# Kernel tuning notes

Measured on AMD Instinct MI355X. Metric: run time of the kernel, lower is better.

Reference implementation:

```python
import jax, jax.numpy as jnp
import numpy as np

NUM_GROUPS = 10
BN_EPS = 1e-5


def _conv1d(x, w, b):
    # x: [B, C, L], w: [O, I, K], 'same' padding
    y = jax.lax.conv_general_dilated(x, w, window_strides=(1,), padding='SAME',
                                     dimension_numbers=('NCH', 'OIH', 'NCH'))
    return y + b[None, :, None]


def _batchnorm1d(x, gamma, beta):
    # training-mode batch statistics over (batch, length) per channel
    mean = jnp.mean(x, axis=(0, 2), keepdims=True)
    var = jnp.var(x, axis=(0, 2), keepdims=True)
    return (x - mean) * jax.lax.rsqrt(var + BN_EPS) * gamma[None, :, None] + beta[None, :, None]


def _conv_block(x, cw, cb, g, b, rw=None, rb=None):
    residual = x if rw is None else _conv1d(x, rw, rb)
    y = jax.nn.relu(_batchnorm1d(_conv1d(x, cw, cb), g, b))
    return y + residual  # dropout is identity at inference


def setup_inputs() -> dict:
    key = jax.random.key(0)
    ks = jax.random.split(key, 16)
    B, N, F, H, G, C = 64, 4096, 512, 64, NUM_GROUPS, 2
    s = lambda k, shp, fan: jax.random.normal(k, shp, jnp.float32) * (1.0 / np.sqrt(fan))
    return {
        'x':    jax.random.normal(ks[0], (B, N, F), jnp.float32),
        'Wd':   s(ks[1], (F, H), F),   'bd':  jnp.zeros((H,), jnp.float32),
        'Wa1':  s(ks[2], (H, H // 2), H), 'ba1': jnp.zeros((H // 2,), jnp.float32),
        'Wa2':  s(ks[3], (H // 2, 1), H // 2), 'ba2': jnp.zeros((1,), jnp.float32),
        'c1w':  s(ks[4], (H, G, 3), G * 3), 'c1b': jnp.zeros((H,), jnp.float32),
        'bn1g': jnp.ones((H,), jnp.float32), 'bn1b': jnp.zeros((H,), jnp.float32),
        'r1w':  s(ks[5], (H, G, 1), G), 'r1b': jnp.zeros((H,), jnp.float32),
        'c2w':  s(ks[6], (H, H, 3), H * 3), 'c2b': jnp.zeros((H,), jnp.float32),
        'bn2g': jnp.ones((H,), jnp.float32), 'bn2b': jnp.zeros((H,), jnp.float32),
        'Wc':   s(ks[7], (H, C), H), 'bc': jnp.zeros((C,), jnp.float32),
    }


def reference(x, Wd, bd, Wa1, ba1, Wa2, ba2, c1w, c1b, bn1g, bn1b, r1w, r1b,
              c2w, c2b, bn2g, bn2b, Wc, bc):
    B, N, _ = x.shape
    h = x @ Wd + bd                                   # [B, N, H]
    # lightweight patch attention
    scores = jnp.tanh(h @ Wa1 + ba1) @ Wa2 + ba2      # [B, N, 1]
    mask = (jnp.sum(jnp.abs(h), axis=2, keepdims=True) > 0).astype(h.dtype)
    scores = scores * mask - 1e10 * (1.0 - mask)
    attn = jax.nn.softmax(scores, axis=1)             # [B, N, 1]
    weighted = h * attn                               # [B, N, H]
    # segment-sum patches into fixed contiguous groups
    ppg = (N + NUM_GROUPS - 1) // NUM_GROUPS
    seg = jnp.arange(N) // ppg                        # [N]
    onehot = jax.nn.one_hot(seg, NUM_GROUPS, dtype=h.dtype)  # [N, G]
    grouped = jnp.einsum('bnh,ng->bgh', weighted, onehot)    # [B, G, H]
    # conv stack on [B, G(channels), H(length)]
    y = _conv_block(grouped, c1w, c1b, bn1g, bn1b, r1w, r1b)
    y = _conv_block(y, c2w, c2b, bn2g, bn2b)
    pooled = jnp.mean(y, axis=2)                      # [B, H] global avg pool
    logits = pooled @ Wc + bc                         # [B, 2]
    return logits
```

## Files before the change

### kernel.cpp

```cpp
#include <hip/hip_runtime.h>
#include <math.h>

#define B_   64
#define N_   4096
#define F_   512
#define H_   64
#define G_   10
#define PPG_ 410

typedef __attribute__((ext_vector_type(8))) short short8v;
typedef __attribute__((ext_vector_type(16))) float f32x16;

__device__ __forceinline__ unsigned short f2bf(float f) {
    union { float f; unsigned int u; } v; v.f = f;
    const unsigned int u = v.u;
    return (unsigned short)((u + 0x7FFFu + ((u >> 16) & 1u)) >> 16);
}
__device__ __forceinline__ float bf2f(unsigned short u) {
    union { unsigned int u; float f; } v; v.u = ((unsigned int)u) << 16;
    return v.f;
}
__device__ __forceinline__ float fast_tanh(float x) {
    return 1.f - 2.f / (__expf(2.f * x) + 1.f);
}

static const size_t OFF_H    = 0;
static const size_t OFF_PNUM = 16777216;
static const size_t OFF_PDEN = OFF_PNUM + 524288;
static const size_t OFF_B1P  = OFF_PDEN + 4096;
static const size_t OFF_B1Q  = OFF_B1P + 4096;
static const size_t OFF_B2P  = OFF_B1Q + 4096;
static const size_t OFF_B2Q  = OFF_B2P + 4096;
static const size_t OFF_Y1   = OFF_B2Q + 4096;
static const size_t OFF_RES1 = OFF_Y1  + 262144;
static const size_t OFF_Z1   = OFF_RES1+ 262144;
static const size_t OFF_Y2   = OFF_Z1  + 262144;
static const size_t OFF_WDT  = OFF_Y2  + 262144;

__global__ __launch_bounds__(256) void k0_wdt(const float* __restrict__ Wd,
                                              unsigned short* __restrict__ WdT)
{
    const int t = blockIdx.x * 256 + threadIdx.x;
    const int k = t >> 6, c = t & 63;
    WdT[((size_t)c << 9) + k] = f2bf(Wd[t]);
}

__global__ __launch_bounds__(256) void k1_gemm(
    const float* __restrict__ x, const unsigned short* __restrict__ WdT,
    const float* __restrict__ bd, unsigned short* __restrict__ h)
{
    __shared__ __align__(16) unsigned char atile[2 * 8192];
    __shared__ __align__(16) unsigned char btile[65536];

    const int tid = threadIdx.x;
    const int w   = tid >> 6;
    const int l   = tid & 63;
    const int rowb = (w >> 1) << 5;
    const int lc  = l & 31;
    const int kh  = l >> 5;

    #pragma unroll
    for (int i = 0; i < 16; ++i) {
        const int p = i * 4096 + tid * 16;
        short8v v = *(const short8v*)((const unsigned char*)WdT + p);
        const int col = p >> 10;
        const int k0  = (p >> 1) & 511;
        const int j   = k0 >> 4;
        const int khh = (k0 >> 3) & 1;
        const int dst = ((j << 1) + (col >> 5)) * 1024 + ((khh << 5) + (col & 31)) * 16;
        *(short8v*)(btile + dst) = v;
    }

    const int srow = tid >> 2;
    const int sq   = tid & 3;
    int wo[4];
    #pragma unroll
    for (int j = 0; j < 4; ++j)
        wo[j] = srow * 128 + ((((j << 1) + (sq >> 1)) ^ (srow & 7)) << 4) + ((sq & 1) << 3);

    const int rb  = (rowb + lc) * 128;
    const int rx7 = lc & 7;
    const unsigned char* bbase = btile + (w & 1) * 1024;

    const int mt0 = blockIdx.x * 8;

    #pragma unroll 1
    for (int mt = 0; mt < 8; ++mt) {
        const int m0 = (mt0 + mt) * 64;
        const float* sp = x + (size_t)(m0 + srow) * F_ + sq * 4;

        f32x16 acc;
        #pragma unroll
        for (int i = 0; i < 16; ++i) acc[i] = 0.f;

        float4 px[4];
        #pragma unroll
        for (int j = 0; j < 4; ++j) px[j] = *(const float4*)(sp + j * 16);
        #pragma unroll
        for (int j = 0; j < 4; ++j) {
            ushort4 v;
            v.x = f2bf(px[j].x); v.y = f2bf(px[j].y);
            v.z = f2bf(px[j].z); v.w = f2bf(px[j].w);
            *(ushort4*)(atile + wo[j]) = v;
        }
        __syncthreads();

        int cur = 0;
        #pragma unroll 1
        for (int t = 0; t < 8; ++t) {
            if (t < 7) {
                const float* q = sp + (t + 1) * 64;
                #pragma unroll
                for (int j = 0; j < 4; ++j) px[j] = *(const float4*)(q + j * 16);
            }
            const unsigned char* ab = atile + cur * 8192;
            #pragma unroll
            for (int s = 0; s < 4; ++s) {
                short8v a = *(const short8v*)(ab + rb + (((kh + 2 * s) ^ rx7) << 4));
                short8v b = *(const short8v*)(bbase + (((t * 4 + s) << 1)) * 1024 + l * 16);
                acc = __builtin_amdgcn_mfma_f32_32x32x16_bf16(a, b, acc, 0, 0, 0);
            }
            if (t < 7) {
                unsigned char* wbuf = atile + (cur ^ 1) * 8192;
                #pragma unroll
                for (int j = 0; j < 4; ++j) {
                    ushort4 v;
                    v.x = f2bf(px[j].x); v.y = f2bf(px[j].y);
                    v.z = f2bf(px[j].z); v.w = f2bf(px[j].w);
                    *(ushort4*)(wbuf + wo[j]) = v;
                }
            }
            __syncthreads();
            cur ^= 1;
        }

        const int col = ((w & 1) << 5) + lc;
        const float bcol = bd[col];
        unsigned short* hb = h + (size_t)m0 * H_;
        #pragma unroll
        for (int r = 0; r < 16; ++r) {
            const int row = rowb + (r & 3) + ((r >> 2) << 3) + (kh << 2);
            hb[(size_t)row * H_ + col] = f2bf(acc[r] + bcol);
        }
    }
}

__global__ __launch_bounds__(256) void k2a_scores(
    const unsigned short* __restrict__ h,
    const float* __restrict__ Wa1, const float* __restrict__ ba1,
    const float* __restrict__ Wa2, const float* __restrict__ ba2,
    float* __restrict__ pnum, float* __restrict__ pden)
{
    __shared__ __align__(16) float rowbuf[64][68];
    __shared__ __align__(16) float was[2048];
    __shared__ float bas[32], wa2s[32];
    __shared__ float sexp[64];
    __shared__ float rnum[4][2][64];

    const int p = blockIdx.x, tid = threadIdx.x;
    for (int i = tid; i < 2048; i += 256) was[i] = Wa1[i];
    if (tid < 32) { bas[tid] = ba1[tid]; wa2s[tid] = Wa2[tid]; }

    const int sr = tid >> 2;
    const int q  = tid & 3;
    const int j0 = q * 8;
    const size_t n0 = (size_t)p * 64;

    {
        const unsigned short* src = h + (n0 + sr) * H_ + q * 16;
        short8v v0 = *(const short8v*)(src);
        short8v v1 = *(const short8v*)(src + 8);
        float* dst = &rowbuf[sr][q * 16];
        float4 f0, f1, f2, f3;
        f0.x = bf2f((unsigned short)v0[0]); f0.y = bf2f((unsigned short)v0[1]);
        f0.z = bf2f((unsigned short)v0[2]); f0.w = bf2f((unsigned short)v0[3]);
        f1.x = bf2f((unsigned short)v0[4]); f1.y = bf2f((unsigned short)v0[5]);
        f1.z = bf2f((unsigned short)v0[6]); f1.w = bf2f((unsigned short)v0[7]);
        f2.x = bf2f((unsigned short)v1[0]); f2.y = bf2f((unsigned short)v1[1]);
        f2.z = bf2f((unsigned short)v1[2]); f2.w = bf2f((unsigned short)v1[3]);
        f3.x = bf2f((unsigned short)v1[4]); f3.y = bf2f((unsigned short)v1[5]);
        f3.z = bf2f((unsigned short)v1[6]); f3.w = bf2f((unsigned short)v1[7]);
        *(float4*)(dst)      = f0;
        *(float4*)(dst + 4)  = f1;
        *(float4*)(dst + 8)  = f2;
        *(float4*)(dst + 12) = f3;
    }
    __syncthreads();

    const float4* was4 = (const float4*)was;
    float tac[8];
    #pragma unroll
    for (int u = 0; u < 8; ++u) tac[u] = bas[j0 + u];
    for (int k = 0; k < 64; ++k) {
        const float hv = rowbuf[sr][k];
        const float4 wa = was4[k * 8 + (q << 1)];
        const float4 wb = was4[k * 8 + (q << 1) + 1];
        tac[0] += hv * wa.x; tac[1] += hv * wa.y;
        tac[2] += hv * wa.z; tac[3] += hv * wa.w;
        tac[4] += hv * wb.x; tac[5] += hv * wb.y;
        tac[6] += hv * wb.z; tac[7] += hv * wb.w;
    }
    float part = 0.f;
    #pragma unroll
    for (int u = 0; u < 8; ++u) part += fast_tanh(tac[u]) * wa2s[j0 + u];
    float sa = 0.f;
    for (int k = q * 16; k < q * 16 + 16; ++k) sa += fabsf(rowbuf[sr][k]);
    part += __shfl_xor(part, 1);
    part += __shfl_xor(part, 2);
    sa   += __shfl_xor(sa, 1);
    sa   += __shfl_xor(sa, 2);
    if (q == 0) sexp[sr] = (sa > 0.f) ? __expf(part + ba2[0]) : 0.f;
    __syncthreads();

    if (tid < 64) {
        float e = sexp[tid];
        #pragma unroll
        for (int o = 1; o < 64; o <<= 1) e += __shfl_xor(e, o);
        if (tid == 0) pden[p] = e;
    }

    const int pl   = p & 63;
    const int nb0  = pl * 64;
    const int glo  = nb0 / PPG_;
    const int col  = tid & 63, qq = tid >> 6;
    float acc0 = 0.f, acc1 = 0.f;
    for (int r = qq; r < 64; r += 4) {
        const float e = sexp[r];
        const float v = rowbuf[r][col];
        if ((nb0 + r) / PPG_ == glo) acc0 += e * v; else acc1 += e * v;
    }
    rnum[qq][0][col] = acc0;
    rnum[qq][1][col] = acc1;
    __syncthreads();
    if (tid < 128) {
        const int slot = tid >> 6, c2 = tid & 63;
        pnum[((size_t)p * 2 + slot) * 64 + c2] =
            rnum[0][slot][c2] + rnum[1][slot][c2] + rnum[2][slot][c2] + rnum[3][slot][c2];
    }
}

__global__ __launch_bounds__(256) void k4_conv1(
    const float* __restrict__ pnum, const float* __restrict__ pden,
    const float* __restrict__ c1w, const float* __restrict__ c1b,
    const float* __restrict__ r1w, const float* __restrict__ r1b,
    float* __restrict__ y1raw, float* __restrict__ res1,
    float* __restrict__ b1p, float* __restrict__ b1q)
{
    __shared__ __align__(16) float gs[G_][68];
    __shared__ float cws[30 * 64];
    __shared__ float rws[G_ * 64];
    __shared__ float c1bs[64], r1bs[64];
    __shared__ float red[256];
    __shared__ float dsh;

    const int b = blockIdx.x, tid = threadIdx.x;

    if (tid < 64) {
        float e = pden[b * 64 + tid];
        #pragma unroll
        for (int o = 1; o < 64; o <<= 1) e += __shfl_xor(e, o);
        if (tid == 0) dsh = e;
    }
    for (int i = tid; i < 30 * 64; i += 256) {
        const int ik = i >> 6, o = i & 63;
        cws[i] = c1w[o * 30 + ik];
    }
    for (int i = tid; i < G_ * 64; i += 256) {
        const int ch = i >> 6, o = i & 63;
        rws[i] = r1w[o * G_ + ch];
    }
    if (tid < 64) { c1bs[tid] = c1b[tid]; r1bs[tid] = r1b[tid]; }
    if (tid < G_) { gs[tid][0] = 0.f; gs[tid][65] = 0.f; gs[tid][66] = 0.f; gs[tid][67] = 0.f; }
    __syncthreads();

    const float inv = 1.f / dsh;
    for (int i = tid; i < 640; i += 256) {
        const int ch = i >> 6, col = i & 63;
        int p_lo = (PPG_ * ch) >> 6;
        int p_hi = (PPG_ * (ch + 1) - 1) >> 6;
        if (p_hi > 63) p_hi = 63;
        float acc = 0.f;
        for (int pl = p_lo; pl <= p_hi; ++pl) {
            const int glo = (pl * 64) / PPG_;
            const int slot = (glo == ch) ? 0 : 1;
            acc += pnum[(((size_t)(b * 64 + pl)) * 2 + slot) * 64 + col];
        }
        gs[ch][1 + col] = acc * inv;
    }
    __syncthreads();

    const int o = tid & 63, lq = tid >> 6;
    float acc[16], racc[16];
    #pragma unroll
    for (int s = 0; s < 16; ++s) { acc[s] = c1bs[o]; racc[s] = r1bs[o]; }

    #pragma unroll
    for (int i = 0; i < G_; ++i) {
        const float* row = &gs[i][lq * 16];
        const float4 a0 = *(const float4*)&row[0];
        const float4 a1 = *(const float4*)&row[4];
        const float4 a2 = *(const float4*)&row[8];
        const float4 a3 = *(const float4*)&row[12];
        const float w16 = row[16], w17 = row[17];
        const float win[18] = { a0.x,a0.y,a0.z,a0.w, a1.x,a1.y,a1.z,a1.w,
                                a2.x,a2.y,a2.z,a2.w, a3.x,a3.y,a3.z,a3.w, w16, w17 };
        const float w0 = cws[(i * 3 + 0) * 64 + o];
        const float w1 = cws[(i * 3 + 1) * 64 + o];
        const float w2 = cws[(i * 3 + 2) * 64 + o];
        const float rw = rws[i * 64 + o];
        #pragma unroll
        for (int s = 0; s < 16; ++s) {
            acc[s]  += win[s] * w0 + win[s + 1] * w1 + win[s + 2] * w2;
            racc[s] += win[s + 1] * rw;
        }
    }

    float psum = 0.f, psq = 0.f;
    #pragma unroll
    for (int s = 0; s < 16; ++s) { psum += acc[s]; psq += acc[s] * acc[s]; }

    float* yo = &y1raw[(size_t)(b * 64 + o) * 64 + lq * 16];
    float* ro = &res1 [(size_t)(b * 64 + o) * 64 + lq * 16];
    #pragma unroll
    for (int s4 = 0; s4 < 4; ++s4) {
        float4 v; v.x = acc[s4*4]; v.y = acc[s4*4+1]; v.z = acc[s4*4+2]; v.w = acc[s4*4+3];
        *(float4*)&yo[s4 * 4] = v;
        float4 u; u.x = racc[s4*4]; u.y = racc[s4*4+1]; u.z = racc[s4*4+2]; u.w = racc[s4*4+3];
        *(float4*)&ro[s4 * 4] = u;
    }
    red[tid] = psum; __syncthreads();
    if (tid < 64) b1p[b * 64 + tid] = red[tid] + red[tid + 64] + red[tid + 128] + red[tid + 192];
    __syncthreads();
    red[tid] = psq; __syncthreads();
    if (tid < 64) b1q[b * 64 + tid] = red[tid] + red[tid + 64] + red[tid + 128] + red[tid + 192];
}

__global__ __launch_bounds__(256) void k5_conv2(
    const float* __restrict__ y1raw, const float* __restrict__ res1,
    const float* __restrict__ b1p, const float* __restrict__ b1q,
    const float* __restrict__ bn1g, const float* __restrict__ bn1b,
    const float* __restrict__ c2w, const float* __restrict__ c2b,
    float* __restrict__ z1, float* __restrict__ y2raw,
    float* __restrict__ b2p, float* __restrict__ b2q)
{
    __shared__ __align__(16) float zs[64][68];
    __shared__ float c2ws[192 * 64];
    __shared__ float s1[64], sh1[64], c2bs[64];
    __shared__ float red[256];

    const int b = blockIdx.x, tid = threadIdx.x;
    if (tid < 64) {
        float sm = 0.f, sq = 0.f;
        for (int blk = 0; blk < 64; ++blk) { sm += b1p[blk * 64 + tid]; sq += b1q[blk * 64 + tid]; }
        const float mean = sm * (1.f / 4096.f);
        const float var  = sq * (1.f / 4096.f) - mean * mean;
        const float sc   = bn1g[tid] * rsqrtf(var + 1e-5f);
        s1[tid] = sc; sh1[tid] = bn1b[tid] - mean * sc;
        zs[tid][0] = 0.f; zs[tid][65] = 0.f;
        c2bs[tid] = c2b[tid];
    }
    for (int i = tid; i < 192 * 64; i += 256) {
        const int ik = i >> 6, o = i & 63;
        c2ws[i] = c2w[o * 192 + ik];
    }
    __syncthreads();
    for (int i = tid; i < 4096; i += 256) {
        const int o = i >> 6, l = i & 63;
        float v = y1raw[(size_t)b * 4096 + i];
        v = fmaxf(0.f, v * s1[o] + sh1[o]) + res1[(size_t)b * 4096 + i];
        z1[(size_t)b * 4096 + i] = v;
        zs[o][1 + l] = v;
    }
    __syncthreads();

    const int o = tid & 63, lq = tid >> 6;
    float acc[16];
    #pragma unroll
    for (int s = 0; s < 16; ++s) acc[s] = c2bs[o];

    #pragma unroll 4
    for (int i = 0; i < 64; ++i) {
        const float* row = &zs[i][lq * 16];
        const float4 a0 = *(const float4*)&row[0];
        const float4 a1 = *(const float4*)&row[4];
        const float4 a2 = *(const float4*)&row[8];
        const float4 a3 = *(const float4*)&row[12];
        const float w16 = row[16], w17 = row[17];
        const float win[18] = { a0.x,a0.y,a0.z,a0.w, a1.x,a1.y,a1.z,a1.w,
                                a2.x,a2.y,a2.z,a2.w, a3.x,a3.y,a3.z,a3.w, w16, w17 };
        const float w0 = c2ws[(i * 3 + 0) * 64 + o];
        const float w1 = c2ws[(i * 3 + 1) * 64 + o];
        const float w2 = c2ws[(i * 3 + 2) * 64 + o];
        #pragma unroll
        for (int s = 0; s < 16; ++s)
            acc[s] += win[s] * w0 + win[s + 1] * w1 + win[s + 2] * w2;
    }

    float psum = 0.f, psq = 0.f;
    #pragma unroll
    for (int s = 0; s < 16; ++s) { psum += acc[s]; psq += acc[s] * acc[s]; }

    float* yo = &y2raw[(size_t)b * 4096 + o * 64 + lq * 16];
    #pragma unroll
    for (int s4 = 0; s4 < 4; ++s4) {
        float4 v; v.x = acc[s4*4]; v.y = acc[s4*4+1]; v.z = acc[s4*4+2]; v.w = acc[s4*4+3];
        *(float4*)&yo[s4 * 4] = v;
    }
    red[tid] = psum; __syncthreads();
    if (tid < 64) b2p[b * 64 + tid] = red[tid] + red[tid + 64] + red[tid + 128] + red[tid + 192];
    __syncthreads();
    red[tid] = psq; __syncthreads();
    if (tid < 64) b2q[b * 64 + tid] = red[tid] + red[tid + 64] + red[tid + 128] + red[tid + 192];
}

__global__ __launch_bounds__(256) void k6_final(
    const float* __restrict__ y2raw, const float* __restrict__ z1,
    const float* __restrict__ b2p, const float* __restrict__ b2q,
    const float* __restrict__ bn2g, const float* __restrict__ bn2b,
    const float* __restrict__ Wc, const float* __restrict__ bc,
    float* __restrict__ out)
{
    __shared__ float s2[64], sh2[64];
    __shared__ float red[256];
    __shared__ float pl[64];
    const int b = blockIdx.x, tid = threadIdx.x;
    if (tid < 64) {
        float sm = 0.f, sq = 0.f;
        for (int blk = 0; blk < 64; ++blk) { sm += b2p[blk * 64 + tid]; sq += b2q[blk * 64 + tid]; }
        const float mean = sm * (1.f / 4096.f);
        const float var  = sq * (1.f / 4096.f) - mean * mean;
        const float sc   = bn2g[tid] * rsqrtf(var + 1e-5f);
        s2[tid] = sc; sh2[tid] = bn2b[tid] - mean * sc;
    }
    __syncthreads();
    const int o = tid & 63, lq = tid >> 6;
    float psum = 0.f;
    for (int s = 0; s < 16; ++s) {
        const int l = lq * 16 + s;
        const size_t idx = (size_t)b * 4096 + o * 64 + l;
        psum += fmaxf(0.f, y2raw[idx] * s2[o] + sh2[o]) + z1[idx];
    }
    red[tid] = psum; __syncthreads();
    if (tid < 64) pl[tid] = (red[tid] + red[tid + 64] + red[tid + 128] + red[tid + 192]) * (1.f / 64.f);
    __syncthreads();
    if (tid < 2) {
        float lg = bc[tid];
        for (int o2 = 0; o2 < 64; ++o2) lg += pl[o2] * Wc[o2 * 2 + tid];
        out[b * 2 + tid] = lg;
    }
}

extern "C" void kernel_launch(void* const* d_in, const int* in_sizes, int n_in,
                              void* d_out, int out_size, void* d_ws, size_t ws_size,
                              hipStream_t stream)
{
    (void)in_sizes; (void)n_in; (void)out_size; (void)ws_size;
    const float* x    = (const float*)d_in[0];
    const float* Wd   = (const float*)d_in[1];
    const float* bd   = (const float*)d_in[2];
    const float* Wa1  = (const float*)d_in[3];
    const float* ba1  = (const float*)d_in[4];
    const float* Wa2  = (const float*)d_in[5];
    const float* ba2  = (const float*)d_in[6];
    const float* c1w  = (const float*)d_in[7];
    const float* c1b  = (const float*)d_in[8];
    const float* bn1g = (const float*)d_in[9];
    const float* bn1b = (const float*)d_in[10];
    const float* r1w  = (const float*)d_in[11];
    const float* r1b  = (const float*)d_in[12];
    const float* c2w  = (const float*)d_in[13];
    const float* c2b  = (const float*)d_in[14];
    const float* bn2g = (const float*)d_in[15];
    const float* bn2b = (const float*)d_in[16];
    const float* Wc   = (const float*)d_in[17];
    const float* bc   = (const float*)d_in[18];

    float* ws      = (float*)d_ws;
    unsigned short* h = (unsigned short*)(ws + OFF_H);
    float* pnum    = ws + OFF_PNUM;
    float* pden    = ws + OFF_PDEN;
    float* b1p     = ws + OFF_B1P;
    float* b1q     = ws + OFF_B1Q;
    float* b2p     = ws + OFF_B2P;
    float* b2q     = ws + OFF_B2Q;
    float* y1raw   = ws + OFF_Y1;
    float* res1    = ws + OFF_RES1;
    float* z1      = ws + OFF_Z1;
    float* y2raw   = ws + OFF_Y2;
    unsigned short* WdT = (unsigned short*)(ws + OFF_WDT);

    k0_wdt<<<dim3(128), dim3(256), 0, stream>>>(Wd, WdT);
    k1_gemm<<<dim3(512), dim3(256), 0, stream>>>(x, WdT, bd, h);
    k2a_scores<<<dim3((B_ * N_) / 64), dim3(256), 0, stream>>>(h, Wa1, ba1, Wa2, ba2, pnum, pden);
    k4_conv1<<<dim3(B_), dim3(256), 0, stream>>>(pnum, pden, c1w, c1b, r1w, r1b,
                                                 y1raw, res1, b1p, b1q);
    k5_conv2<<<dim3(B_), dim3(256), 0, stream>>>(y1raw, res1, b1p, b1q, bn1g, bn1b,
                                                 c2w, c2b, z1, y2raw, b2p, b2q);
    k6_final<<<dim3(B_), dim3(256), 0, stream>>>(y2raw, z1, b2p, b2q, bn2g, bn2b,
                                                 Wc, bc, (float*)d_out);
}
```

Before: 188.7 us.

## Fuse conv stack kernels into one with grid barriers and shared-memory intermediates

Merges the three small per-batch conv/BN/pool kernels into a single 64-block kernel that uses an atomic grid barrier for the batch-norm statistics. Intermediate activations (y1, residual, z1, y2) now stay in LDS instead of round-tripping through global memory. This removes two kernel launches and the global traffic, at the cost of a memset launch, a spin-wait barrier that relies on all 64 blocks being co-resident, and much higher LDS use per block.

```diff
diff --git a/kernel.cpp b/kernel.cpp
--- a/kernel.cpp
+++ b/kernel.cpp
@@ -31,11 +31,8 @@
 static const size_t OFF_B1Q  = OFF_B1P + 4096;
 static const size_t OFF_B2P  = OFF_B1Q + 4096;
 static const size_t OFF_B2Q  = OFF_B2P + 4096;
-static const size_t OFF_Y1   = OFF_B2Q + 4096;
-static const size_t OFF_RES1 = OFF_Y1  + 262144;
-static const size_t OFF_Z1   = OFF_RES1+ 262144;
-static const size_t OFF_Y2   = OFF_Z1  + 262144;
-static const size_t OFF_WDT  = OFF_Y2  + 262144;
+static const size_t OFF_WDT  = OFF_B2Q + 4096;
+static const size_t OFF_BAR  = OFF_WDT + 16384;
 
 __global__ __launch_bounds__(256) void k0_wdt(const float* __restrict__ Wd,
                                               unsigned short* __restrict__ WdT)
@@ -239,38 +236,66 @@
     }
 }
 
-__global__ __launch_bounds__(256) void k4_conv1(
+__device__ __forceinline__ void grid_barrier(unsigned int* bar, int idx) {
+    __syncthreads();
+    __threadfence();
+    if (threadIdx.x == 0) {
+        __hip_atomic_fetch_add(&bar[idx], 1u, __ATOMIC_ACQ_REL, __HIP_MEMORY_SCOPE_AGENT);
+        while (__hip_atomic_load(&bar[idx], __ATOMIC_ACQUIRE, __HIP_MEMORY_SCOPE_AGENT)
+               < (unsigned)B_) {
+            __builtin_amdgcn_s_sleep(8);
+        }
+    }
+    __syncthreads();
+    __threadfence();
+}
+
+__global__ __launch_bounds__(256) void k456_convstack(
     const float* __restrict__ pnum, const float* __restrict__ pden,
     const float* __restrict__ c1w, const float* __restrict__ c1b,
     const float* __restrict__ r1w, const float* __restrict__ r1b,
-    float* __restrict__ y1raw, float* __restrict__ res1,
-    float* __restrict__ b1p, float* __restrict__ b1q)
+    const float* __restrict__ bn1g, const float* __restrict__ bn1b,
+    const float* __restrict__ c2w, const float* __restrict__ c2b,
+    const float* __restrict__ bn2g, const float* __restrict__ bn2b,
+    const float* __restrict__ Wc, const float* __restrict__ bc,
+    float* __restrict__ b1p, float* __restrict__ b1q,
+    float* __restrict__ b2p, float* __restrict__ b2q,
+    unsigned int* __restrict__ bar, float* __restrict__ out)
 {
     __shared__ __align__(16) float gs[G_][68];
     __shared__ float cws[30 * 64];
     __shared__ float rws[G_ * 64];
     __shared__ float c1bs[64], r1bs[64];
+    __shared__ __align__(16) float y1s[64 * 68];
+    __shared__ __align__(16) float r1s[64 * 68];
+    __shared__ __align__(16) float zs[64][68];
+    __shared__ float c2ws[192 * 64];
+    __shared__ float s1[64], sh1[64], c2bs[64];
+    __shared__ float s2[64], sh2[64];
     __shared__ float red[256];
+    __shared__ float plv[64];
     __shared__ float dsh;
 
     const int b = blockIdx.x, tid = threadIdx.x;
+    const int o = tid & 63, lq = tid >> 6;
 
     if (tid < 64) {
         float e = pden[b * 64 + tid];
         #pragma unroll
-        for (int o = 1; o < 64; o <<= 1) e += __shfl_xor(e, o);
+        for (int oo = 1; oo < 64; oo <<= 1) e += __shfl_xor(e, oo);
         if (tid == 0) dsh = e;
     }
     for (int i = tid; i < 30 * 64; i += 256) {
-        const int ik = i >> 6, o = i & 63;
-        cws[i] = c1w[o * 30 + ik];
+        const int ik = i >> 6, oo = i & 63;
+        cws[i] = c1w[oo * 30 + ik];
     }
     for (int i = tid; i < G_ * 64; i += 256) {
-        const int ch = i >> 6, o = i & 63;
-        rws[i] = r1w[o * G_ + ch];
+        const int ch = i >> 6, oo = i & 63;
+        rws[i] = r1w[oo * G_ + ch];
     }
     if (tid < 64) { c1bs[tid] = c1b[tid]; r1bs[tid] = r1b[tid]; }
     if (tid < G_) { gs[tid][0] = 0.f; gs[tid][65] = 0.f; gs[tid][66] = 0.f; gs[tid][67] = 0.f; }
+    if (tid < 64) { zs[tid][0] = 0.f; zs[tid][65] = 0.f; }
     __syncthreads();
 
     const float inv = 1.f / dsh;
@@ -289,66 +314,51 @@
     }
     __syncthreads();
 
-    const int o = tid & 63, lq = tid >> 6;
-    float acc[16], racc[16];
-    #pragma unroll
-    for (int s = 0; s < 16; ++s) { acc[s] = c1bs[o]; racc[s] = r1bs[o]; }
-
-    #pragma unroll
-    for (int i = 0; i < G_; ++i) {
-        const float* row = &gs[i][lq * 16];
-        const float4 a0 = *(const float4*)&row[0];
-        const float4 a1 = *(const float4*)&row[4];
-        const float4 a2 = *(const float4*)&row[8];
-        const float4 a3 = *(const float4*)&row[12];
-        const float w16 = row[16], w17 = row[17];
-        const float win[18] = { a0.x,a0.y,a0.z,a0.w, a1.x,a1.y,a1.z,a1.w,
-                                a2.x,a2.y,a2.z,a2.w, a3.x,a3.y,a3.z,a3.w, w16, w17 };
-        const float w0 = cws[(i * 3 + 0) * 64 + o];
-        const float w1 = cws[(i * 3 + 1) * 64 + o];
-        const float w2 = cws[(i * 3 + 2) * 64 + o];
-        const float rw = rws[i * 64 + o];
-        #pragma unroll
-        for (int s = 0; s < 16; ++s) {
-            acc[s]  += win[s] * w0 + win[s + 1] * w1 + win[s + 2] * w2;
-            racc[s] += win[s + 1] * rw;
-        }
-    }
-
-    float psum = 0.f, psq = 0.f;
-    #pragma unroll
-    for (int s = 0; s < 16; ++s) { psum += acc[s]; psq += acc[s] * acc[s]; }
-
-    float* yo = &y1raw[(size_t)(b * 64 + o) * 64 + lq * 16];
-    float* ro = &res1 [(size_t)(b * 64 + o) * 64 + lq * 16];
-    #pragma unroll
-    for (int s4 = 0; s4 < 4; ++s4) {
-        float4 v; v.x = acc[s4*4]; v.y = acc[s4*4+1]; v.z = acc[s4*4+2]; v.w = acc[s4*4+3];
-        *(float4*)&yo[s4 * 4] = v;
-        float4 u; u.x = racc[s4*4]; u.y = racc[s4*4+1]; u.z = racc[s4*4+2]; u.w = racc[s4*4+3];
-        *(float4*)&ro[s4 * 4] = u;
-    }
-    red[tid] = psum; __syncthreads();
-    if (tid < 64) b1p[b * 64 + tid] = red[tid] + red[tid + 64] + red[tid + 128] + red[tid + 192];
-    __syncthreads();
-    red[tid] = psq; __syncthreads();
-    if (tid < 64) b1q[b * 64 + tid] = red[tid] + red[tid + 64] + red[tid + 128] + red[tid + 192];
-}
-
-__global__ __launch_bounds__(256) void k5_conv2(
-    const float* __restrict__ y1raw, const float* __restrict__ res1,
-    const float* __restrict__ b1p, const float* __restrict__ b1q,
-    const float* __restrict__ bn1g, const float* __restrict__ bn1b,
-    const float* __restrict__ c2w, const float* __restrict__ c2b,
-    float* __restrict__ z1, float* __restrict__ y2raw,
-    float* __restrict__ b2p, float* __restrict__ b2q)
-{
-    __shared__ __align__(16) float zs[64][68];
-    __shared__ float c2ws[192 * 64];
-    __shared__ float s1[64], sh1[64], c2bs[64];
-    __shared__ float red[256];
-
-    const int b = blockIdx.x, tid = threadIdx.x;
+    {
+        float acc[16], racc[16];
+        #pragma unroll
+        for (int s = 0; s < 16; ++s) { acc[s] = c1bs[o]; racc[s] = r1bs[o]; }
+        #pragma unroll
+        for (int i = 0; i < G_; ++i) {
+            const float* row = &gs[i][lq * 16];
+            const float4 a0 = *(const float4*)&row[0];
+            const float4 a1 = *(const float4*)&row[4];
+            const float4 a2 = *(const float4*)&row[8];
+            const float4 a3 = *(const float4*)&row[12];
+            const float w16 = row[16], w17 = row[17];
+            const float win[18] = { a0.x,a0.y,a0.z,a0.w, a1.x,a1.y,a1.z,a1.w,
+                                    a2.x,a2.y,a2.z,a2.w, a3.x,a3.y,a3.z,a3.w, w16, w17 };
+            const float w0 = cws[(i * 3 + 0) * 64 + o];
+            const float w1 = cws[(i * 3 + 1) * 64 + o];
+            const float w2 = cws[(i * 3 + 2) * 64 + o];
+            const float rw = rws[i * 64 + o];
+            #pragma unroll
+            for (int s = 0; s < 16; ++s) {
+                acc[s]  += win[s] * w0 + win[s + 1] * w1 + win[s + 2] * w2;
+                racc[s] += win[s + 1] * rw;
+            }
+        }
+        float psum = 0.f, psq = 0.f;
+        #pragma unroll
+        for (int s = 0; s < 16; ++s) { psum += acc[s]; psq += acc[s] * acc[s]; }
+        float* yo = &y1s[o * 68 + lq * 16];
+        float* ro = &r1s[o * 68 + lq * 16];
+        #pragma unroll
+        for (int s4 = 0; s4 < 4; ++s4) {
+            float4 v; v.x = acc[s4*4]; v.y = acc[s4*4+1]; v.z = acc[s4*4+2]; v.w = acc[s4*4+3];
+            *(float4*)&yo[s4 * 4] = v;
+            float4 u; u.x = racc[s4*4]; u.y = racc[s4*4+1]; u.z = racc[s4*4+2]; u.w = racc[s4*4+3];
+            *(float4*)&ro[s4 * 4] = u;
+        }
+        red[tid] = psum; __syncthreads();
+        if (tid < 64) b1p[b * 64 + tid] = red[tid] + red[tid + 64] + red[tid + 128] + red[tid + 192];
+        __syncthreads();
+        red[tid] = psq; __syncthreads();
+        if (tid < 64) b1q[b * 64 + tid] = red[tid] + red[tid + 64] + red[tid + 128] + red[tid + 192];
+    }
+
+    grid_barrier(bar, 0);
+
     if (tid < 64) {
         float sm = 0.f, sq = 0.f;
         for (int blk = 0; blk < 64; ++blk) { sm += b1p[blk * 64 + tid]; sq += b1q[blk * 64 + tid]; }
@@ -356,74 +366,61 @@
         const float var  = sq * (1.f / 4096.f) - mean * mean;
         const float sc   = bn1g[tid] * rsqrtf(var + 1e-5f);
         s1[tid] = sc; sh1[tid] = bn1b[tid] - mean * sc;
-        zs[tid][0] = 0.f; zs[tid][65] = 0.f;
         c2bs[tid] = c2b[tid];
     }
     for (int i = tid; i < 192 * 64; i += 256) {
-        const int ik = i >> 6, o = i & 63;
-        c2ws[i] = c2w[o * 192 + ik];
+        const int ik = i >> 6, oo = i & 63;
+        c2ws[i] = c2w[oo * 192 + ik];
     }
     __syncthreads();
     for (int i = tid; i < 4096; i += 256) {
-        const int o = i >> 6, l = i & 63;
-        float v = y1raw[(size_t)b * 4096 + i];
-        v = fmaxf(0.f, v * s1[o] + sh1[o]) + res1[(size_t)b * 4096 + i];
-        z1[(size_t)b * 4096 + i] = v;
-        zs[o][1 + l] = v;
-    }
-    __syncthreads();
-
-    const int o = tid & 63, lq = tid >> 6;
-    float acc[16];
-    #pragma unroll
-    for (int s = 0; s < 16; ++s) acc[s] = c2bs[o];
-
-    #pragma unroll 4
-    for (int i = 0; i < 64; ++i) {
-        const float* row = &zs[i][lq * 16];
-        const float4 a0 = *(const float4*)&row[0];
-        const float4 a1 = *(const float4*)&row[4];
-        const float4 a2 = *(const float4*)&row[8];
-        const float4 a3 = *(const float4*)&row[12];
-        const float w16 = row[16], w17 = row[17];
-        const float win[18] = { a0.x,a0.y,a0.z,a0.w, a1.x,a1.y,a1.z,a1.w,
-                                a2.x,a2.y,a2.z,a2.w, a3.x,a3.y,a3.z,a3.w, w16, w17 };
-        const float w0 = c2ws[(i * 3 + 0) * 64 + o];
-        const float w1 = c2ws[(i * 3 + 1) * 64 + o];
-        const float w2 = c2ws[(i * 3 + 2) * 64 + o];
-        #pragma unroll
-        for (int s = 0; s < 16; ++s)
-            acc[s] += win[s] * w0 + win[s + 1] * w1 + win[s + 2] * w2;
-    }
-
-    float psum = 0.f, psq = 0.f;
-    #pragma unroll
-    for (int s = 0; s < 16; ++s) { psum += acc[s]; psq += acc[s] * acc[s]; }
-
-    float* yo = &y2raw[(size_t)b * 4096 + o * 64 + lq * 16];
-    #pragma unroll
-    for (int s4 = 0; s4 < 4; ++s4) {
-        float4 v; v.x = acc[s4*4]; v.y = acc[s4*4+1]; v.z = acc[s4*4+2]; v.w = acc[s4*4+3];
-        *(float4*)&yo[s4 * 4] = v;
-    }
-    red[tid] = psum; __syncthreads();
-    if (tid < 64) b2p[b * 64 + tid] = red[tid] + red[tid + 64] + red[tid + 128] + red[tid + 192];
-    __syncthreads();
-    red[tid] = psq; __syncthreads();
-    if (tid < 64) b2q[b * 64 + tid] = red[tid] + red[tid + 64] + red[tid + 128] + red[tid + 192];
-}
-
-__global__ __launch_bounds__(256) void k6_final(
-    const float* __restrict__ y2raw, const float* __restrict__ z1,
-    const float* __restrict__ b2p, const float* __restrict__ b2q,
-    const float* __restrict__ bn2g, const float* __restrict__ bn2b,
-    const float* __restrict__ Wc, const float* __restrict__ bc,
-    float* __restrict__ out)
-{
-    __shared__ float s2[64], sh2[64];
-    __shared__ float red[256];
-    __shared__ float pl[64];
-    const int b = blockIdx.x, tid = threadIdx.x;
+        const int oo = i >> 6, l = i & 63;
+        float v = y1s[oo * 68 + l];
+        v = fmaxf(0.f, v * s1[oo] + sh1[oo]) + r1s[oo * 68 + l];
+        zs[oo][1 + l] = v;
+    }
+    __syncthreads();
+
+    {
+        float acc[16];
+        #pragma unroll
+        for (int s = 0; s < 16; ++s) acc[s] = c2bs[o];
+        #pragma unroll 4
+        for (int i = 0; i < 64; ++i) {
+            const float* row = &zs[i][lq * 16];
+            const float4 a0 = *(const float4*)&row[0];
+            const float4 a1 = *(const float4*)&row[4];
+            const float4 a2 = *(const float4*)&row[8];
+            const float4 a3 = *(const float4*)&row[12];
+            const float w16 = row[16], w17 = row[17];
+            const float win[18] = { a0.x,a0.y,a0.z,a0.w, a1.x,a1.y,a1.z,a1.w,
+                                    a2.x,a2.y,a2.z,a2.w, a3.x,a3.y,a3.z,a3.w, w16, w17 };
+            const float w0 = c2ws[(i * 3 + 0) * 64 + o];
+            const float w1 = c2ws[(i * 3 + 1) * 64 + o];
+            const float w2 = c2ws[(i * 3 + 2) * 64 + o];
+            #pragma unroll
+            for (int s = 0; s < 16; ++s)
+                acc[s] += win[s] * w0 + win[s + 1] * w1 + win[s + 2] * w2;
+        }
+        float psum = 0.f, psq = 0.f;
+        #pragma unroll
+        for (int s = 0; s < 16; ++s) { psum += acc[s]; psq += acc[s] * acc[s]; }
+        __syncthreads();
+        float* yo = &y1s[o * 68 + lq * 16];
+        #pragma unroll
+        for (int s4 = 0; s4 < 4; ++s4) {
+            float4 v; v.x = acc[s4*4]; v.y = acc[s4*4+1]; v.z = acc[s4*4+2]; v.w = acc[s4*4+3];
+            *(float4*)&yo[s4 * 4] = v;
+        }
+        red[tid] = psum; __syncthreads();
+        if (tid < 64) b2p[b * 64 + tid] = red[tid] + red[tid + 64] + red[tid + 128] + red[tid + 192];
+        __syncthreads();
+        red[tid] = psq; __syncthreads();
+        if (tid < 64) b2q[b * 64 + tid] = red[tid] + red[tid + 64] + red[tid + 128] + red[tid + 192];
+    }
+
+    grid_barrier(bar, 1);
+
     if (tid < 64) {
         float sm = 0.f, sq = 0.f;
         for (int blk = 0; blk < 64; ++blk) { sm += b2p[blk * 64 + tid]; sq += b2q[blk * 64 + tid]; }
@@ -433,19 +430,18 @@
         s2[tid] = sc; sh2[tid] = bn2b[tid] - mean * sc;
     }
     __syncthreads();
-    const int o = tid & 63, lq = tid >> 6;
     float psum = 0.f;
+    #pragma unroll
     for (int s = 0; s < 16; ++s) {
         const int l = lq * 16 + s;
-        const size_t idx = (size_t)b * 4096 + o * 64 + l;
-        psum += fmaxf(0.f, y2raw[idx] * s2[o] + sh2[o]) + z1[idx];
+        psum += fmaxf(0.f, y1s[o * 68 + l] * s2[o] + sh2[o]) + zs[o][1 + l];
     }
     red[tid] = psum; __syncthreads();
-    if (tid < 64) pl[tid] = (red[tid] + red[tid + 64] + red[tid + 128] + red[tid + 192]) * (1.f / 64.f);
+    if (tid < 64) plv[tid] = (red[tid] + red[tid + 64] + red[tid + 128] + red[tid + 192]) * (1.f / 64.f);
     __syncthreads();
     if (tid < 2) {
         float lg = bc[tid];
-        for (int o2 = 0; o2 < 64; ++o2) lg += pl[o2] * Wc[o2 * 2 + tid];
+        for (int o2 = 0; o2 < 64; ++o2) lg += plv[o2] * Wc[o2 * 2 + tid];
         out[b * 2 + tid] = lg;
     }
 }
@@ -483,19 +479,15 @@
     float* b1q     = ws + OFF_B1Q;
     float* b2p     = ws + OFF_B2P;
     float* b2q     = ws + OFF_B2Q;
-    float* y1raw   = ws + OFF_Y1;
-    float* res1    = ws + OFF_RES1;
-    float* z1      = ws + OFF_Z1;
-    float* y2raw   = ws + OFF_Y2;
     unsigned short* WdT = (unsigned short*)(ws + OFF_WDT);
+    unsigned int* bar   = (unsigned int*)(ws + OFF_BAR);
+
+    hipMemsetAsync(bar, 0, 2 * sizeof(unsigned int), stream);
 
     k0_wdt<<<dim3(128), dim3(256), 0, stream>>>(Wd, WdT);
     k1_gemm<<<dim3(512), dim3(256), 0, stream>>>(x, WdT, bd, h);
     k2a_scores<<<dim3((B_ * N_) / 64), dim3(256), 0, stream>>>(h, Wa1, ba1, Wa2, ba2, pnum, pden);
-    k4_conv1<<<dim3(B_), dim3(256), 0, stream>>>(pnum, pden, c1w, c1b, r1w, r1b,
-                                                 y1raw, res1, b1p, b1q);
-    k5_conv2<<<dim3(B_), dim3(256), 0, stream>>>(y1raw, res1, b1p, b1q, bn1g, bn1b,
-                                                 c2w, c2b, z1, y2raw, b2p, b2q);
-    k6_final<<<dim3(B_), dim3(256), 0, stream>>>(y2raw, z1, b2p, b2q, bn2g, bn2b,
-                                                 Wc, bc, (float*)d_out);
-}
+    k456_convstack<<<dim3(B_), dim3(256), 0, stream>>>(
+        pnum, pden, c1w, c1b, r1w, r1b, bn1g, bn1b, c2w, c2b, bn2g, bn2b,
+        Wc, bc, b1p, b1q, b2p, b2q, bar, (float*)d_out);
+}
```

Result: slower. 207.3 us (+9.8%).
